# Optimization experiments

Measured on AMD Instinct MI355X. Metric: run time of the kernel, lower is better.

Reference implementation:

```python
import jax, jax.numpy as jnp
import numpy as np

Q_DIM = 512
K_DIM = 512
HID = 512


def setup_inputs() -> dict:
    key = jax.random.key(0)
    k1, k2, k3, k4, k5, k6 = jax.random.split(key, 6)
    b, n_q, s = 4, 64, 1024
    queries = jax.random.normal(k1, (b, n_q, Q_DIM), dtype=jnp.float32)
    keys = jax.random.normal(k2, (b, s, K_DIM), dtype=jnp.float32)
    values = jax.random.normal(k3, (b, s, 512), dtype=jnp.float32)
    lim1 = 1.0 / np.sqrt(Q_DIM + K_DIM)
    W1 = jax.random.uniform(k4, (HID, Q_DIM + K_DIM), minval=-lim1, maxval=lim1, dtype=jnp.float32)
    b1 = jax.random.uniform(k5, (HID,), minval=-lim1, maxval=lim1, dtype=jnp.float32)
    lim2 = 1.0 / np.sqrt(HID)
    w2 = jax.random.uniform(k6, (HID,), minval=-lim2, maxval=lim2, dtype=jnp.float32)
    return {"queries": queries, "keys": keys, "values": values,
            "W1": W1, "b1": b1, "w2": w2}


def reference(queries, keys, values, W1, b1, w2):
    # linear1 on concat([q, k]) == W1q @ q + W1k @ k (split the weight),
    # avoiding materializing the concatenated [b, n_q, s, q_v+k_v] tensor.
    W1q = W1[:, :Q_DIM]  # [hid, q_dim]
    W1k = W1[:, Q_DIM:]  # [hid, k_dim]
    q_proj = jnp.einsum('bqd,hd->bqh', queries, W1q)          # [b, n_q, hid]
    k_proj = jnp.einsum('bsd,hd->bsh', keys, W1k) + b1        # [b, s, hid]
    hidden = jnp.tanh(q_proj[:, :, None, :] + k_proj[:, None, :, :])  # [b, n_q, s, hid]
    scores = jnp.einsum('bqsh,h->bqs', hidden, w2)            # [b, n_q, s]
    attn = jax.nn.softmax(scores, axis=2)                     # softmax over key axis
    final = jnp.einsum('bqs,bsv->bqv', attn, values)          # [b, n_q, v_dim]
    return final
```

## Files before the change

kernel.cpp:

```cpp
#include <hip/hip_runtime.h>


static constexpr int SLEN = 1024;
static constexpr int DIM  = 512;
static constexpr float TANH_SCALE = 2.885390081777927f;

typedef __attribute__((ext_vector_type(8))) short bf16x8;
typedef __attribute__((ext_vector_type(4))) float f32x4;

__device__ __forceinline__ float fast_exp2(float x) { return __builtin_amdgcn_exp2f(x); }
__device__ __forceinline__ float fast_rcp(float x)  { return __builtin_amdgcn_rcpf(x); }

__device__ __forceinline__ unsigned int f2bf(float f) {
    unsigned int u = __float_as_uint(f);
    u += 0x7FFF + ((u >> 16) & 1);
    return u >> 16;
}

__device__ __forceinline__ void async_copy16(const void* g, void* l) {
    __builtin_amdgcn_global_load_lds(
        (const __attribute__((address_space(1))) unsigned int*)g,
        (__attribute__((address_space(3))) unsigned int*)l, 16, 0, 0);
}

__global__ __launch_bounds__(256) void convert_bf16(
    const float* __restrict__ q, const float* __restrict__ k,
    const float* __restrict__ w, unsigned short* __restrict__ qb,
    unsigned short* __restrict__ kb, unsigned short* __restrict__ wb)
{
    int id = blockIdx.x * 256 + threadIdx.x;
    const float* src; unsigned short* dst; int off;
    if (id < 32768)        { src = q; dst = qb; off = id; }
    else if (id < 557056)  { src = k; dst = kb; off = id - 32768; }
    else                   { src = w; dst = wb; off = id - 557056; }
    float4 v = ((const float4*)src)[off];
    ushort4 o;
    o.x = (unsigned short)f2bf(v.x); o.y = (unsigned short)f2bf(v.y);
    o.z = (unsigned short)f2bf(v.z); o.w = (unsigned short)f2bf(v.w);
    ((ushort4*)dst)[off] = o;
}

__global__ __launch_bounds__(256) void proj_mfma(
    const unsigned short* __restrict__ qb, const unsigned short* __restrict__ kb,
    const unsigned short* __restrict__ wb, const float* __restrict__ b1,
    float* __restrict__ qp, float* __restrict__ kp)
{
    __shared__ __align__(16) unsigned short As[64][64];
    __shared__ __align__(16) unsigned short Ws[64][64];

    const int bx = blockIdx.x;
    const unsigned short* A; float* C; const float* bias; int mb, nb, col_off;
    if (bx < 512) {
        A = kb; C = kp; bias = b1; col_off = 512;
        mb = (bx >> 3) * 64; nb = (bx & 7) * 64;
    } else {
        int b2 = bx - 512;
        A = qb; C = qp; bias = nullptr; col_off = 0;
        mb = (b2 >> 3) * 64; nb = (b2 & 7) * 64;
    }

    const int t = threadIdx.x;
    const int l = t & 63;
    const int wv = t >> 6;
    const int wm = (wv & 1) * 32;
    const int wn = (wv >> 1) * 32;
    const int lane16 = l & 15;
    const int quad   = l >> 4;
    const int r8   = l >> 3;
    const int schk = (l & 7) ^ r8;

    f32x4 acc[2][2] = {{{0.f,0.f,0.f,0.f},{0.f,0.f,0.f,0.f}},
                       {{0.f,0.f,0.f,0.f},{0.f,0.f,0.f,0.f}}};

    for (int kc = 0; kc < DIM; kc += 64) {
#pragma unroll
        for (int i = 0; i < 2; ++i) {
            int rbase = wv * 16 + i * 8;
            async_copy16(A + (size_t)(mb + rbase + r8) * DIM + kc + schk * 8, &As[rbase][0]);
            async_copy16(wb + (size_t)(nb + rbase + r8) * 1024 + col_off + kc + schk * 8, &Ws[rbase][0]);
        }
        __syncthreads();

#pragma unroll
        for (int ks = 0; ks < 2; ++ks) {
            int cc = ks * 4 + quad;
            int sw = (cc ^ (lane16 & 7)) << 3;
            bf16x8 a0  = *(const bf16x8*)&As[wm + lane16][sw];
            bf16x8 a1  = *(const bf16x8*)&As[wm + 16 + lane16][sw];
            bf16x8 b0  = *(const bf16x8*)&Ws[wn + lane16][sw];
            bf16x8 b1v = *(const bf16x8*)&Ws[wn + 16 + lane16][sw];
            acc[0][0] = __builtin_amdgcn_mfma_f32_16x16x32_bf16(a0, b0,  acc[0][0], 0, 0, 0);
            acc[0][1] = __builtin_amdgcn_mfma_f32_16x16x32_bf16(a0, b1v, acc[0][1], 0, 0, 0);
            acc[1][0] = __builtin_amdgcn_mfma_f32_16x16x32_bf16(a1, b0,  acc[1][0], 0, 0, 0);
            acc[1][1] = __builtin_amdgcn_mfma_f32_16x16x32_bf16(a1, b1v, acc[1][1], 0, 0, 0);
        }
        __syncthreads();
    }

#pragma unroll
    for (int mi = 0; mi < 2; ++mi) {
#pragma unroll
        for (int ni = 0; ni < 2; ++ni) {
            int col = nb + wn + 16 * ni + lane16;
            float bv = bias ? bias[col] : 0.0f;
#pragma unroll
            for (int r = 0; r < 4; ++r) {
                int row = mb + wm + 16 * mi + quad * 4 + r;
                C[(size_t)row * DIM + col] = (acc[mi][ni][r] + bv) * TANH_SCALE;
            }
        }
    }
}

__global__ __launch_bounds__(256) void scores_kernel(
    const float* __restrict__ qp, const float* __restrict__ kp,
    const float* __restrict__ w2, float* __restrict__ th)
{
    __shared__ __align__(16) float qs[16][68];
    __shared__ __align__(16) float ks[32][68];
    __shared__ __align__(16) float ws2[256];
    const int t     = threadIdx.x;
    const int sb    = blockIdx.x * 32;
    const int qt    = blockIdx.y & 3;
    const int half  = blockIdx.y >> 2;
    const int kbase = half * 256;
    const int qrow0 = blockIdx.z * 64 + qt * 16;
    const int krow0 = blockIdx.z * 1024 + sb;
    float* thh = th + (size_t)half * 256 * SLEN;

    if (t < 64) *(float4*)&ws2[t << 2] = *(const float4*)(w2 + kbase + (t << 2));

    const int tq = t >> 4;
    const int ts = t & 15;
    float a00 = 0.f, a01 = 0.f, a10 = 0.f, a11 = 0.f;

    for (int kc = 0; kc < 256; kc += 64) {
        {
            int r = t >> 4, g = (t & 15) << 2;
            *(float4*)&qs[r][g] = *(const float4*)(qp + (size_t)(qrow0 + r) * DIM + kbase + kc + g);
        }
#pragma unroll
        for (int rr = 0; rr < 2; ++rr) {
            int idx = t + rr * 256;
            int r = idx >> 4, g = (idx & 15) << 2;
            *(float4*)&ks[r][g] = *(const float4*)(kp + (size_t)(krow0 + r) * DIM + kbase + kc + g);
        }
        __syncthreads();
#pragma unroll
        for (int k4 = 0; k4 < 16; ++k4) {
            float4 qv = *(const float4*)&qs[tq][k4 << 2];
            float4 k0 = *(const float4*)&ks[ts][k4 << 2];
            float4 k1 = *(const float4*)&ks[ts + 16][k4 << 2];
            float4 wv = *(const float4*)&ws2[kc + (k4 << 2)];
            {
                float dx = 1.0f + fast_exp2(qv.x + k0.x);
                float dy = 1.0f + fast_exp2(qv.y + k0.y);
                float num = fmaf(wv.y, dx, wv.x * dy);
                a00 = fmaf(num, fast_rcp(dx * dy), a00);
            }
            {
                float dz = 1.0f + fast_exp2(qv.z + k0.z);
                float dw = 1.0f + fast_exp2(qv.w + k0.w);
                float num = fmaf(wv.w, dz, wv.z * dw);
                a01 = fmaf(num, fast_rcp(dz * dw), a01);
            }
            {
                float dx = 1.0f + fast_exp2(qv.x + k1.x);
                float dy = 1.0f + fast_exp2(qv.y + k1.y);
                float num = fmaf(wv.y, dx, wv.x * dy);
                a10 = fmaf(num, fast_rcp(dx * dy), a10);
            }
            {
                float dz = 1.0f + fast_exp2(qv.z + k1.z);
                float dw = 1.0f + fast_exp2(qv.w + k1.w);
                float num = fmaf(wv.w, dz, wv.z * dw);
                a11 = fmaf(num, fast_rcp(dz * dw), a11);
            }
        }
        __syncthreads();
    }
    thh[(size_t)(qrow0 + tq) * SLEN + sb + ts]      = -TANH_SCALE * (a00 + a01);
    thh[(size_t)(qrow0 + tq) * SLEN + sb + ts + 16] = -TANH_SCALE * (a10 + a11);
}

__global__ __launch_bounds__(256) void av_gemm(
    const float* __restrict__ th, const float* __restrict__ values,
    float* __restrict__ pt, float* __restrict__ sums_p)
{
    __shared__ __align__(16) float As[32][68];
    __shared__ __align__(16) float Bs[32][68];
    const int t  = threadIdx.x;
    const int nb = blockIdx.x * 64;
    const int kt = blockIdx.y;
    const int kb = kt * 128;
    const int b  = blockIdx.z;
    const int tx = t & 15, ty = t >> 4;
    float acc[4][4] = {};
    float rsum[2] = {0.f, 0.f};
    for (int kc = 0; kc < 128; kc += 32) {
        const int k0 = kb + kc;
#pragma unroll
        for (int r = 0; r < 2; ++r) {
            int idx = t + r * 256;
            int m   = idx >> 3;
            int k4  = (idx & 7) << 2;
            size_t base = (size_t)(b * 64 + m) * SLEN + k0 + k4;
            float4 t0 = *(const float4*)(th + base);
            float4 t1 = *(const float4*)(th + 262144 + base);
            float4 e;
            e.x = fast_exp2(t0.x + t1.x);
            e.y = fast_exp2(t0.y + t1.y);
            e.z = fast_exp2(t0.z + t1.z);
            e.w = fast_exp2(t0.w + t1.w);
            As[k4 + 0][m] = e.x; As[k4 + 1][m] = e.y;
            As[k4 + 2][m] = e.z; As[k4 + 3][m] = e.w;
            rsum[r] += e.x + e.y + e.z + e.w;
            int kk = idx >> 4;
            int g  = (idx & 15) << 2;
            *(float4*)&Bs[kk][g] =
                *(const float4*)(values + (size_t)(b * 1024 + k0 + kk) * DIM + nb + g);
        }
        __syncthreads();
#pragma unroll
        for (int k = 0; k < 32; ++k) {
            float4 a  = *(const float4*)&As[k][ty << 2];
            float4 bv = *(const float4*)&Bs[k][tx << 2];
            float am[4] = {a.x, a.y, a.z, a.w};
            float bn[4] = {bv.x, bv.y, bv.z, bv.w};
#pragma unroll
            for (int i = 0; i < 4; ++i)
#pragma unroll
                for (int j = 0; j < 4; ++j)
                    acc[i][j] = fmaf(am[i], bn[j], acc[i][j]);
        }
        __syncthreads();
    }
#pragma unroll
    for (int i = 0; i < 4; ++i) {
        int row = b * 64 + (ty << 2) + i;
        float4 o;
        o.x = acc[i][0]; o.y = acc[i][1]; o.z = acc[i][2]; o.w = acc[i][3];
        *(float4*)(pt + ((size_t)kt * 256 + row) * DIM + nb + (tx << 2)) = o;
    }
    if (nb == 0) {
#pragma unroll
        for (int r = 0; r < 2; ++r) {
            float v = rsum[r];
            v += __shfl_xor(v, 1, 64);
            v += __shfl_xor(v, 2, 64);
            v += __shfl_xor(v, 4, 64);
            if ((t & 7) == 0) {
                int m = (t >> 3) + r * 32;
                sums_p[kt * 256 + b * 64 + m] = v;
            }
        }
    }
}

__global__ __launch_bounds__(256) void reduce_kernel(
    const float* __restrict__ pt, const float* __restrict__ sums_p,
    float* __restrict__ out)
{
    int idx = blockIdx.x * 256 + threadIdx.x;
    const float4* p = (const float4*)pt;
    float4 a = p[idx];
#pragma unroll
    for (int k = 1; k < 8; ++k) {
        float4 v = p[k * 32768 + idx];
        a.x += v.x; a.y += v.y; a.z += v.z; a.w += v.w;
    }
    int row = idx >> 7;
    float s = 0.f;
#pragma unroll
    for (int k = 0; k < 8; ++k) s += sums_p[k * 256 + row];
    float r = fast_rcp(s);
    a.x *= r; a.y *= r; a.z *= r; a.w *= r;
    ((float4*)out)[idx] = a;
}

extern "C" void kernel_launch(void* const* d_in, const int* in_sizes, int n_in,
                              void* d_out, int out_size, void* d_ws, size_t ws_size,
                              hipStream_t stream) {
    const float* queries = (const float*)d_in[0];
    const float* keys    = (const float*)d_in[1];
    const float* values  = (const float*)d_in[2];
    const float* W1      = (const float*)d_in[3];
    const float* b1      = (const float*)d_in[4];
    const float* w2      = (const float*)d_in[5];
    float* out = (float*)d_out;

    float* qp     = (float*)d_ws;
    float* kp     = qp + 131072;
    float* th     = kp + 2097152;
    float* pt     = th + 2 * 262144;
    float* sums_p = pt + 8 * 131072;
    unsigned short* qbf = (unsigned short*)(sums_p + 2048);
    unsigned short* kbf = qbf + 131072;
    unsigned short* wbf = kbf + 2097152;
    (void)in_sizes; (void)n_in; (void)ws_size; (void)out_size;

    convert_bf16<<<dim3(2688), 256, 0, stream>>>(queries, keys, W1, qbf, kbf, wbf);
    proj_mfma<<<dim3(544), 256, 0, stream>>>(qbf, kbf, wbf, b1, qp, kp);
    scores_kernel<<<dim3(32, 8, 4), 256, 0, stream>>>(qp, kp, w2, th);
    av_gemm<<<dim3(8, 8, 4), 256, 0, stream>>>(th, values, pt, sums_p);
    reduce_kernel<<<dim3(128), 256, 0, stream>>>(pt, sums_p, out);
}
```

Before: 122.7 us.

## Precompute exp2 of projections so the scores loop uses products instead of exps

The projection GEMM epilogue now stores exp2 of the scaled projections instead of the scaled values. The pairwise scores loop can then form 1+exp2(q+k) as fma(q_exp, k_exp, 1), removing one transcendental per (q, s, h) element from the hot loop. The exps are paid once per projection element instead. This risks overflow or inf for large pre-activations, since exp2 of the scaled values is stored in fp32 and multiplied.

```diff
diff --git a/kernel.cpp b/kernel.cpp
--- a/kernel.cpp
+++ b/kernel.cpp
@@ -106,7 +106,7 @@
 #pragma unroll
             for (int r = 0; r < 4; ++r) {
                 int row = mb + wm + 16 * mi + quad * 4 + r;
-                C[(size_t)row * DIM + col] = (acc[mi][ni][r] + bv) * TANH_SCALE;
+                C[(size_t)row * DIM + col] = fast_exp2((acc[mi][ni][r] + bv) * TANH_SCALE);
             }
         }
     }
@@ -153,28 +153,20 @@
             float4 k1 = *(const float4*)&ks[ts + 16][k4 << 2];
             float4 wv = *(const float4*)&ws2[kc + (k4 << 2)];
             {
-                float dx = 1.0f + fast_exp2(qv.x + k0.x);
-                float dy = 1.0f + fast_exp2(qv.y + k0.y);
-                float num = fmaf(wv.y, dx, wv.x * dy);
-                a00 = fmaf(num, fast_rcp(dx * dy), a00);
+                float d0 = fmaf(qv.x, k0.x, 1.0f);
+                float d1 = fmaf(qv.y, k0.y, 1.0f);
+                a00 = fmaf(fmaf(wv.x, d1, wv.y * d0), fast_rcp(d0 * d1), a00);
+                float d2 = fmaf(qv.z, k0.z, 1.0f);
+                float d3 = fmaf(qv.w, k0.w, 1.0f);
+                a01 = fmaf(fmaf(wv.z, d3, wv.w * d2), fast_rcp(d2 * d3), a01);
             }
             {
-                float dz = 1.0f + fast_exp2(qv.z + k0.z);
-                float dw = 1.0f + fast_exp2(qv.w + k0.w);
-                float num = fmaf(wv.w, dz, wv.z * dw);
-                a01 = fmaf(num, fast_rcp(dz * dw), a01);
-            }
-            {
-                float dx = 1.0f + fast_exp2(qv.x + k1.x);
-                float dy = 1.0f + fast_exp2(qv.y + k1.y);
-                float num = fmaf(wv.y, dx, wv.x * dy);
-                a10 = fmaf(num, fast_rcp(dx * dy), a10);
-            }
-            {
-                float dz = 1.0f + fast_exp2(qv.z + k1.z);
-                float dw = 1.0f + fast_exp2(qv.w + k1.w);
-                float num = fmaf(wv.w, dz, wv.z * dw);
-                a11 = fmaf(num, fast_rcp(dz * dw), a11);
+                float d0 = fmaf(qv.x, k1.x, 1.0f);
+                float d1 = fmaf(qv.y, k1.y, 1.0f);
+                a10 = fmaf(fmaf(wv.x, d1, wv.y * d0), fast_rcp(d0 * d1), a10);
+                float d2 = fmaf(qv.z, k1.z, 1.0f);
+                float d3 = fmaf(qv.w, k1.w, 1.0f);
+                a11 = fmaf(fmaf(wv.z, d3, wv.w * d2), fast_rcp(d2 * d3), a11);
             }
         }
         __syncthreads();
```

Result: faster. 118.3 us (-3.6%).
